# Optimization experiments

Measured on AMD Instinct MI355X. Metric: run time of the kernel, lower is better.

Reference implementation:

```python
import jax, jax.numpy as jnp
import numpy as np

N, S, H = 100000, 150, 150
G = 4  # gates: input, output, forget, update


def setup_inputs() -> dict:
    key = jax.random.key(0)
    ks = jax.random.split(key, 10)
    scale = 1.0 / np.sqrt(H)
    return {
        "s_in": jax.random.normal(ks[0], (N, S), jnp.float32),
        "s_out": jax.random.normal(ks[1], (N, S), jnp.float32),
        "h_in": jax.random.normal(ks[2], (N, H), jnp.float32),
        "h_out": jax.random.normal(ks[3], (N, H), jnp.float32),
        "last_c": jax.random.normal(ks[4], (N, H), jnp.float32),
        "w_in": jax.random.normal(ks[5], (G, S, H), jnp.float32) * scale,
        "w_out": jax.random.normal(ks[6], (G, S, H), jnp.float32) * scale,
        "u_in": jax.random.normal(ks[7], (G, H, H), jnp.float32) * scale,
        "u_out": jax.random.normal(ks[8], (G, H, H), jnp.float32) * scale,
        "b": jax.random.normal(ks[9], (G, H), jnp.float32) * scale,
    }


def reference(s_in, s_out, h_in, h_out, last_c, w_in, w_out, u_in, u_out, b):
    # gates[g] = sigmoid(s_in @ w_in[g] + s_out @ w_out[g] + h_in @ u_in[g]
    #                    + h_out @ u_out[g] + b[g])   -> shape [G, N, H]
    pre = (jnp.einsum("ns,gsh->gnh", s_in, w_in)
           + jnp.einsum("ns,gsh->gnh", s_out, w_out)
           + jnp.einsum("nh,ghk->gnk", h_in, u_in)
           + jnp.einsum("nh,ghk->gnk", h_out, u_out)
           + b[:, None, :])
    gates = jax.nn.sigmoid(pre)
    input_gate, output_gate, forget_gate, update_gate = gates
    cell_state = forget_gate * last_c + update_gate * input_gate
    hidden_state = output_gate * jnp.tanh(cell_state)
    return hidden_state, cell_state
```

## Files before the change

kernel.cpp:

```cpp
#include <hip/hip_runtime.h>
#include <stdint.h>

#define NROWS 100000
#define SDIM 150
#define HDIM 150
#define KSEG 160
#define NKB 20
#define NCOL 640
#define BM 96
#define NTHREADS 768
#define BSLICE 40960
#define ASLICE 6144
#define BUFBYTES (BSLICE + ASLICE)
#define EPI_STRIDE 648

using half8  = __attribute__((ext_vector_type(8))) _Float16;
using half2v = __attribute__((ext_vector_type(2))) _Float16;
using floatx4 = __attribute__((ext_vector_type(4))) float;

__device__ __forceinline__ float fsig(float x) {
  return __builtin_amdgcn_rcpf(1.0f + __expf(-x));
}
__device__ __forceinline__ float ftanh(float x) {
  return 2.0f * __builtin_amdgcn_rcpf(1.0f + __expf(-2.0f * x)) - 1.0f;
}

__device__ __forceinline__ void gload_lds16(const void* g, void* l) {
  __builtin_amdgcn_global_load_lds(
      (const __attribute__((address_space(1))) void*)g,
      (__attribute__((address_space(3))) void*)l, 16, 0, 0);
}

#define KBAR(VM)                                              \
  do {                                                        \
    asm volatile("s_waitcnt vmcnt(" #VM ")" ::: "memory");    \
    asm volatile("s_waitcnt lgkmcnt(0)" ::: "memory");        \
    __builtin_amdgcn_s_barrier();                             \
    asm volatile("" ::: "memory");                            \
  } while (0)

__global__ void pack_w_kernel(const float* __restrict__ w_in,
                              const float* __restrict__ w_out,
                              const float* __restrict__ u_in,
                              const float* __restrict__ u_out,
                              _Float16* __restrict__ wblk) {
  int idx = blockIdx.x * 256 + threadIdx.x;
  if (idx >= NKB * NCOL * 32) return;
  int j    = idx & 7;
  int slot = (idx >> 3) & 3;
  int col  = (idx >> 5) % NCOL;
  int kb   = idx / (NCOL * 32);
  int kg   = slot ^ ((col >> 1) & 3);
  int k    = kb * 32 + kg * 8 + j;
  int seg  = k / KSEG;
  int kl   = k - seg * KSEG;
  int g    = col / KSEG;
  int h    = col - g * KSEG;
  float v = 0.0f;
  if (kl < SDIM && h < HDIM) {
    const float* src = (seg == 0) ? w_in : (seg == 1) ? w_out
                     : (seg == 2) ? u_in : u_out;
    v = src[(g * SDIM + kl) * HDIM + h];
  }
  wblk[idx] = (_Float16)v;
}

__global__ __launch_bounds__(NTHREADS) void lstm_fused_kernel(
    const float* __restrict__ s_in, const float* __restrict__ s_out,
    const float* __restrict__ h_in, const float* __restrict__ h_out,
    const float* __restrict__ last_c, const float* __restrict__ bias,
    const _Float16* __restrict__ wblk,
    float* __restrict__ out_hid, float* __restrict__ out_cell) {
  __shared__ __align__(16) char lds[3 * BUFBYTES];

  const int tid  = threadIdx.x;
  const int lane = tid & 63;
  const int l15  = lane & 15;
  const int kgrp = lane >> 4;
  const int wid  = tid >> 6;
  const int rgrp = wid >> 2;
  const int gate = wid & 3;
  const int row0 = blockIdx.x * BM;

  const float* segp[4] = {s_in, s_out, h_in, h_out};

  floatx4 acc[2][10] = {};

  const int a_row  = tid >> 3;
  const int a_o    = tid & 7;
  const long n_a   = (long)row0 + a_row;
  const bool a_ok  = (n_a < NROWS);
  const int a_off  = a_row * 64 + (((a_o >> 1) ^ (a_row & 3)) * 16) + (a_o & 1) * 8;

  char* buf0 = lds;
  char* buf1 = lds + BUFBYTES;
  char* buf2 = lds + 2 * BUFBYTES;

  auto stageB = [&](int kb, char* buf) {
    const char* g = (const char*)wblk + (size_t)kb * BSLICE;
    gload_lds16(g + (size_t)tid * 16,          buf + tid * 16);
    gload_lds16(g + (size_t)(tid + 768) * 16,  buf + (tid + 768) * 16);
    gload_lds16(g + (size_t)(tid + 1536) * 16, buf + (tid + 1536) * 16);
    if (tid < 256)
      gload_lds16(g + (size_t)(tid + 2304) * 16, buf + (tid + 2304) * 16);
  };
  auto loadA = [&](int kb, float& v0, float& v1, float& v2, float& v3) {
    v0 = v1 = v2 = v3 = 0.f;
    const int seg = kb / 5;
    const int kls = (kb % 5) * 32 + a_o * 4;
    if (a_ok && kls < SDIM) {
      const float* p = segp[seg] + (size_t)n_a * SDIM + kls;
      float2 q0 = *(const float2*)p;
      v0 = q0.x; v1 = q0.y;
      if (kls + 3 < SDIM) {
        float2 q1 = *(const float2*)(p + 2);
        v2 = q1.x; v3 = q1.y;
      }
    }
  };
  auto commitA = [&](char* buf, float v0, float v1, float v2, float v3) {
    union { _Float16 h[4]; uint2 u; } pk;
    pk.h[0] = (_Float16)v0; pk.h[1] = (_Float16)v1;
    pk.h[2] = (_Float16)v2; pk.h[3] = (_Float16)v3;
    *(uint2*)(buf + BSLICE + a_off) = pk.u;
  };
  auto compute = [&](const char* bc) {
    const char* aB = bc + BSLICE;
    const int r0 = rgrp * 32 + l15;
    half8 af0 = *(const half8*)(aB + r0 * 64 + ((kgrp ^ (r0 & 3)) * 16));
    const int r1 = r0 + 16;
    half8 af1 = *(const half8*)(aB + r1 * 64 + ((kgrp ^ (r1 & 3)) * 16));
#pragma unroll
    for (int ct = 0; ct < 10; ++ct) {
      int col = gate * 160 + ct * 16 + l15;
      half8 bf = *(const half8*)(bc + col * 64 + ((kgrp ^ ((col >> 1) & 3)) * 16));
      acc[0][ct] = __builtin_amdgcn_mfma_f32_16x16x32_f16(af0, bf, acc[0][ct], 0, 0, 0);
      acc[1][ct] = __builtin_amdgcn_mfma_f32_16x16x32_f16(af1, bf, acc[1][ct], 0, 0, 0);
    }
  };

  float an0 = 0.f, an1 = 0.f, an2 = 0.f, an3 = 0.f;
  {
    float a0, a1, a2, a3;
    stageB(0, buf0); loadA(0, a0, a1, a2, a3);
    stageB(1, buf1); loadA(1, an0, an1, an2, an3);
    commitA(buf0, a0, a1, a2, a3);
    if (wid < 4) KBAR(6); else KBAR(5);
  }

  char* bc = buf0;
  char* bn = buf1;
  char* bs = buf2;
#pragma unroll 1
  for (int t = 0; t < NKB; ++t) {
    float av0 = 0.f, av1 = 0.f, av2 = 0.f, av3 = 0.f;
    const bool has2 = (t + 2 < NKB);
    if (has2) {
      stageB(t + 2, bs);
      loadA(t + 2, av0, av1, av2, av3);
    }
    if (t + 1 < NKB) commitA(bn, an0, an1, an2, an3);
    compute(bc);
    an0 = av0; an1 = av1; an2 = av2; an3 = av3;
    if (has2) { if (wid < 4) KBAR(6); else KBAR(5); }
    else      { KBAR(0); }
    char* tmp = bc; bc = bn; bn = bs; bs = tmp;
  }

  float bfrag[10];
#pragma unroll
  for (int ct = 0; ct < 10; ++ct) {
    int h = ct * 16 + l15;
    bfrag[ct] = (h < HDIM) ? bias[gate * HDIM + h] : 0.f;
  }
  _Float16* epi = (_Float16*)lds;
  for (int s = 0; s < 3; ++s) {
    if (s) __syncthreads();
    if (rgrp == s) {
#pragma unroll
      for (int mt = 0; mt < 2; ++mt) {
#pragma unroll
        for (int ct = 0; ct < 10; ++ct) {
          int colb = gate * 160 + ct * 16 + l15;
#pragma unroll
          for (int i = 0; i < 4; ++i) {
            int rl = mt * 16 + kgrp * 4 + i;
            float gv = fsig(acc[mt][ct][i] + bfrag[ct]);
            epi[rl * EPI_STRIDE + colb] = (_Float16)gv;
          }
        }
      }
    }
    __syncthreads();
#pragma unroll
    for (int it = 0; it < 4; ++it) {
      int idx = tid + it * NTHREADS;
      if (idx < 32 * 75) {
        int row = idx / 75;
        int h2  = idx - row * 75;
        long n = (long)row0 + s * 32 + row;
        if (n < NROWS) {
          int h = h2 * 2;
          const _Float16* er = epi + row * EPI_STRIDE + h;
          half2v gi = *(const half2v*)(er + 0 * 160);
          half2v go = *(const half2v*)(er + 1 * 160);
          half2v gf = *(const half2v*)(er + 2 * 160);
          half2v gu = *(const half2v*)(er + 3 * 160);
          float2 lc = *(const float2*)(last_c + n * HDIM + h);
          float c0 = (float)gf[0] * lc.x + (float)gu[0] * (float)gi[0];
          float c1 = (float)gf[1] * lc.y + (float)gu[1] * (float)gi[1];
          float hd0 = (float)go[0] * ftanh(c0);
          float hd1 = (float)go[1] * ftanh(c1);
          *(float2*)(out_hid  + n * HDIM + h) = make_float2(hd0, hd1);
          *(float2*)(out_cell + n * HDIM + h) = make_float2(c0, c1);
        }
      }
    }
  }
}

extern "C" void kernel_launch(void* const* d_in, const int* in_sizes, int n_in,
                              void* d_out, int out_size, void* d_ws, size_t ws_size,
                              hipStream_t stream) {
  const float* s_in   = (const float*)d_in[0];
  const float* s_out  = (const float*)d_in[1];
  const float* h_in   = (const float*)d_in[2];
  const float* h_out  = (const float*)d_in[3];
  const float* last_c = (const float*)d_in[4];
  const float* w_in   = (const float*)d_in[5];
  const float* w_out  = (const float*)d_in[6];
  const float* u_in   = (const float*)d_in[7];
  const float* u_out  = (const float*)d_in[8];
  const float* b      = (const float*)d_in[9];

  _Float16* wblk = (_Float16*)d_ws;

  pack_w_kernel<<<(NKB * NCOL * 32 + 255) / 256, 256, 0, stream>>>(
      w_in, w_out, u_in, u_out, wblk);

  float* out_hid  = (float*)d_out;
  float* out_cell = out_hid + (size_t)NROWS * HDIM;

  lstm_fused_kernel<<<(NROWS + BM - 1) / BM, NTHREADS, 0, stream>>>(
      s_in, s_out, h_in, h_out, last_c, b, wblk, out_hid, out_cell);
}
```

Before: 255.0 us.

## Retile LSTM GEMM to 128-row blocks with 8 waves each owning 80 columns

Changes the block tile from 96 rows with 12 waves to 128 rows with 8 waves, where each wave covers all 128 rows for an 80-column slice, so it holds 8x5 accumulators and reuses each B fragment across 8 row tiles. A loads become 16-byte float4 pairs with a new swizzle, B staging is restructured into 5 loads per thread, the bias load is hoisted, and launch bounds request 2 blocks per CU. The aim is to cut LDS fragment traffic per MFMA and raise arithmetic intensity. The cost is higher register pressure from 160 accumulator floats, which may force spills or lower occupancy.

```diff
diff --git a/kernel.cpp b/kernel.cpp
--- a/kernel.cpp
+++ b/kernel.cpp
@@ -7,12 +7,12 @@
 #define KSEG 160
 #define NKB 20
 #define NCOL 640
-#define BM 96
-#define NTHREADS 768
+#define BM 128
+#define NTHREADS 512
 #define BSLICE 40960
-#define ASLICE 6144
+#define ASLICE 8192
 #define BUFBYTES (BSLICE + ASLICE)
-#define EPI_STRIDE 648
+#define EPI_STRIDE 656
 
 using half8  = __attribute__((ext_vector_type(8))) _Float16;
 using half2v = __attribute__((ext_vector_type(2))) _Float16;
@@ -65,7 +65,7 @@
   wblk[idx] = (_Float16)v;
 }
 
-__global__ __launch_bounds__(NTHREADS) void lstm_fused_kernel(
+__global__ __launch_bounds__(NTHREADS, 2) void lstm_fused_kernel(
     const float* __restrict__ s_in, const float* __restrict__ s_out,
     const float* __restrict__ h_in, const float* __restrict__ h_out,
     const float* __restrict__ last_c, const float* __restrict__ bias,
@@ -78,74 +78,91 @@
   const int l15  = lane & 15;
   const int kgrp = lane >> 4;
   const int wid  = tid >> 6;
-  const int rgrp = wid >> 2;
-  const int gate = wid & 3;
+  const int gate = wid >> 1;
+  const int cb   = wid * 80;
   const int row0 = blockIdx.x * BM;
 
   const float* segp[4] = {s_in, s_out, h_in, h_out};
 
-  floatx4 acc[2][10] = {};
-
-  const int a_row  = tid >> 3;
-  const int a_o    = tid & 7;
-  const long n_a   = (long)row0 + a_row;
-  const bool a_ok  = (n_a < NROWS);
-  const int a_off  = a_row * 64 + (((a_o >> 1) ^ (a_row & 3)) * 16) + (a_o & 1) * 8;
+  floatx4 acc[8][5] = {};
+
+  float bfrag[5];
+#pragma unroll
+  for (int n = 0; n < 5; ++n) {
+    int h = (wid & 1) * 80 + n * 16 + l15;
+    bfrag[n] = (h < HDIM) ? bias[gate * HDIM + h] : 0.f;
+  }
+
+  const int a_row = tid >> 2;
+  const int a_q   = tid & 3;
+  const long n_a  = (long)row0 + a_row;
+  const bool a_ok = (n_a < NROWS);
+  const int a_off = a_row * 64 + ((a_q ^ ((a_row >> 1) & 3)) * 16);
 
   char* buf0 = lds;
   char* buf1 = lds + BUFBYTES;
   char* buf2 = lds + 2 * BUFBYTES;
 
   auto stageB = [&](int kb, char* buf) {
-    const char* g = (const char*)wblk + (size_t)kb * BSLICE;
-    gload_lds16(g + (size_t)tid * 16,          buf + tid * 16);
-    gload_lds16(g + (size_t)(tid + 768) * 16,  buf + (tid + 768) * 16);
-    gload_lds16(g + (size_t)(tid + 1536) * 16, buf + (tid + 1536) * 16);
-    if (tid < 256)
-      gload_lds16(g + (size_t)(tid + 2304) * 16, buf + (tid + 2304) * 16);
-  };
-  auto loadA = [&](int kb, float& v0, float& v1, float& v2, float& v3) {
-    v0 = v1 = v2 = v3 = 0.f;
+    const char* g = (const char*)wblk + (size_t)kb * BSLICE + tid * 16;
+    char* d = buf + tid * 16;
+#pragma unroll
+    for (int i = 0; i < 5; ++i)
+      gload_lds16(g + i * 8192, d + i * 8192);
+  };
+  auto loadA = [&](int kb, float4& lo, float4& hi) {
+    lo = make_float4(0.f, 0.f, 0.f, 0.f);
+    hi = make_float4(0.f, 0.f, 0.f, 0.f);
     const int seg = kb / 5;
-    const int kls = (kb % 5) * 32 + a_o * 4;
+    const int kls = (kb % 5) * 32 + a_q * 8;
     if (a_ok && kls < SDIM) {
       const float* p = segp[seg] + (size_t)n_a * SDIM + kls;
-      float2 q0 = *(const float2*)p;
-      v0 = q0.x; v1 = q0.y;
-      if (kls + 3 < SDIM) {
-        float2 q1 = *(const float2*)(p + 2);
-        v2 = q1.x; v3 = q1.y;
+      if (kls + 7 < SDIM) {
+        lo = *(const float4*)p;
+        hi = *(const float4*)(p + 4);
+      } else {
+        float t[8] = {0.f, 0.f, 0.f, 0.f, 0.f, 0.f, 0.f, 0.f};
+#pragma unroll
+        for (int i = 0; i < 8; ++i)
+          if (kls + i < SDIM) t[i] = p[i];
+        lo = make_float4(t[0], t[1], t[2], t[3]);
+        hi = make_float4(t[4], t[5], t[6], t[7]);
       }
     }
   };
-  auto commitA = [&](char* buf, float v0, float v1, float v2, float v3) {
-    union { _Float16 h[4]; uint2 u; } pk;
-    pk.h[0] = (_Float16)v0; pk.h[1] = (_Float16)v1;
-    pk.h[2] = (_Float16)v2; pk.h[3] = (_Float16)v3;
-    *(uint2*)(buf + BSLICE + a_off) = pk.u;
-  };
-  auto compute = [&](const char* bc) {
-    const char* aB = bc + BSLICE;
-    const int r0 = rgrp * 32 + l15;
-    half8 af0 = *(const half8*)(aB + r0 * 64 + ((kgrp ^ (r0 & 3)) * 16));
-    const int r1 = r0 + 16;
-    half8 af1 = *(const half8*)(aB + r1 * 64 + ((kgrp ^ (r1 & 3)) * 16));
-#pragma unroll
-    for (int ct = 0; ct < 10; ++ct) {
-      int col = gate * 160 + ct * 16 + l15;
-      half8 bf = *(const half8*)(bc + col * 64 + ((kgrp ^ ((col >> 1) & 3)) * 16));
-      acc[0][ct] = __builtin_amdgcn_mfma_f32_16x16x32_f16(af0, bf, acc[0][ct], 0, 0, 0);
-      acc[1][ct] = __builtin_amdgcn_mfma_f32_16x16x32_f16(af1, bf, acc[1][ct], 0, 0, 0);
-    }
-  };
-
-  float an0 = 0.f, an1 = 0.f, an2 = 0.f, an3 = 0.f;
+  auto commitA = [&](char* buf, float4 lo, float4 hi) {
+    union { _Float16 h[8]; uint4 u; } pk;
+    pk.h[0] = (_Float16)lo.x; pk.h[1] = (_Float16)lo.y;
+    pk.h[2] = (_Float16)lo.z; pk.h[3] = (_Float16)lo.w;
+    pk.h[4] = (_Float16)hi.x; pk.h[5] = (_Float16)hi.y;
+    pk.h[6] = (_Float16)hi.z; pk.h[7] = (_Float16)hi.w;
+    *(uint4*)(buf + BSLICE + a_off) = pk.u;
+  };
+  auto compute = [&](const char* bufc) {
+    const char* aB = bufc + BSLICE;
+    half8 bf[5];
+#pragma unroll
+    for (int n = 0; n < 5; ++n) {
+      int col = cb + n * 16 + l15;
+      bf[n] = *(const half8*)(bufc + col * 64 + ((kgrp ^ ((col >> 1) & 3)) * 16));
+    }
+#pragma unroll
+    for (int mt = 0; mt < 8; ++mt) {
+      int r = mt * 16 + l15;
+      half8 af = *(const half8*)(aB + r * 64 + ((kgrp ^ ((r >> 1) & 3)) * 16));
+#pragma unroll
+      for (int n = 0; n < 5; ++n)
+        acc[mt][n] = __builtin_amdgcn_mfma_f32_16x16x32_f16(af, bf[n], acc[mt][n], 0, 0, 0);
+    }
+  };
+
+  float4 anl, anh;
   {
-    float a0, a1, a2, a3;
-    stageB(0, buf0); loadA(0, a0, a1, a2, a3);
-    stageB(1, buf1); loadA(1, an0, an1, an2, an3);
-    commitA(buf0, a0, a1, a2, a3);
-    if (wid < 4) KBAR(6); else KBAR(5);
+    float4 a0l, a0h;
+    stageB(0, buf0); loadA(0, a0l, a0h);
+    stageB(1, buf1); loadA(1, anl, anh);
+    commitA(buf0, a0l, a0h);
+    KBAR(7);
   }
 
   char* bc = buf0;
@@ -153,47 +170,40 @@
   char* bs = buf2;
 #pragma unroll 1
   for (int t = 0; t < NKB; ++t) {
-    float av0 = 0.f, av1 = 0.f, av2 = 0.f, av3 = 0.f;
+    float4 avl, avh;
     const bool has2 = (t + 2 < NKB);
     if (has2) {
       stageB(t + 2, bs);
-      loadA(t + 2, av0, av1, av2, av3);
-    }
-    if (t + 1 < NKB) commitA(bn, an0, an1, an2, an3);
+      loadA(t + 2, avl, avh);
+    }
+    if (t + 1 < NKB) commitA(bn, anl, anh);
     compute(bc);
-    an0 = av0; an1 = av1; an2 = av2; an3 = av3;
-    if (has2) { if (wid < 4) KBAR(6); else KBAR(5); }
-    else      { KBAR(0); }
+    anl = avl; anh = avh;
+    if (has2) KBAR(7); else KBAR(0);
     char* tmp = bc; bc = bn; bn = bs; bs = tmp;
   }
 
-  float bfrag[10];
-#pragma unroll
-  for (int ct = 0; ct < 10; ++ct) {
-    int h = ct * 16 + l15;
-    bfrag[ct] = (h < HDIM) ? bias[gate * HDIM + h] : 0.f;
-  }
   _Float16* epi = (_Float16*)lds;
-  for (int s = 0; s < 3; ++s) {
+#pragma unroll
+  for (int s = 0; s < 4; ++s) {
     if (s) __syncthreads();
-    if (rgrp == s) {
-#pragma unroll
-      for (int mt = 0; mt < 2; ++mt) {
-#pragma unroll
-        for (int ct = 0; ct < 10; ++ct) {
-          int colb = gate * 160 + ct * 16 + l15;
-#pragma unroll
-          for (int i = 0; i < 4; ++i) {
-            int rl = mt * 16 + kgrp * 4 + i;
-            float gv = fsig(acc[mt][ct][i] + bfrag[ct]);
-            epi[rl * EPI_STRIDE + colb] = (_Float16)gv;
-          }
+#pragma unroll
+    for (int mt2 = 0; mt2 < 2; ++mt2) {
+      const int mt = 2 * s + mt2;
+#pragma unroll
+      for (int n = 0; n < 5; ++n) {
+        int col = cb + n * 16 + l15;
+#pragma unroll
+        for (int i = 0; i < 4; ++i) {
+          int rl = mt2 * 16 + kgrp * 4 + i;
+          float gv = fsig(acc[mt][n][i] + bfrag[n]);
+          epi[rl * EPI_STRIDE + col] = (_Float16)gv;
         }
       }
     }
     __syncthreads();
 #pragma unroll
-    for (int it = 0; it < 4; ++it) {
+    for (int it = 0; it < 5; ++it) {
       int idx = tid + it * NTHREADS;
       if (idx < 32 * 75) {
         int row = idx / 75;
```

Result: no change. 251.5 us (-1.4%).
